# Optimization experiments

Measured on AMD Instinct MI355X. Metric: run time of the kernel, lower is better.

The kernel has to match this reference:

```python
import jax, jax.numpy as jnp
import numpy as np

N_NODES = 50000


def sage_conv(x, edge_index, W_l, b_l, W_r):
    # PyG SAGEConv (mean aggr): out_i = lin_l(mean_{j->i} x_j) + lin_r(x_i)
    src, dst = edge_index[0], edge_index[1]
    msgs = x[src]                                        # [E, C] gather
    summed = jax.ops.segment_sum(msgs, dst, num_segments=N_NODES)  # [N, C]
    deg = jax.ops.segment_sum(jnp.ones((edge_index.shape[1],), x.dtype), dst,
                              num_segments=N_NODES)
    mean = summed / jnp.maximum(deg, 1.0)[:, None]
    return mean @ W_l + b_l + x @ W_r


def setup_inputs() -> dict:
    key = jax.random.key(0)
    ks = jax.random.split(key, 12)
    E, EL, C, X = 800000, 1000000, 128, 384
    return {
        "x": jax.random.normal(ks[0], (N_NODES, X), jnp.float32),
        "edge_index": jax.random.randint(ks[1], (2, E), 0, N_NODES),
        "edge_label_index": jax.random.randint(ks[2], (2, EL), 0, N_NODES),
        "W_lin": jax.random.normal(ks[3], (X, C), jnp.float32) * 0.05,
        "b_lin": jax.random.normal(ks[4], (C,), jnp.float32) * 0.05,
        "W1_l": jax.random.normal(ks[5], (C, C), jnp.float32) * 0.08,
        "b1": jax.random.normal(ks[6], (C,), jnp.float32) * 0.05,
        "W1_r": jax.random.normal(ks[7], (C, C), jnp.float32) * 0.08,
        "W2_l": jax.random.normal(ks[8], (C, C), jnp.float32) * 0.08,
        "b2": jax.random.normal(ks[9], (C,), jnp.float32) * 0.05,
        "W2_r": jax.random.normal(ks[10], (C, C), jnp.float32) * 0.08,
    }


def reference(x, edge_index, edge_label_index, W_lin, b_lin,
              W1_l, b1, W1_r, W2_l, b2, W2_r):
    h = x @ W_lin + b_lin                                # label_lin
    h = jax.nn.relu(sage_conv(h, edge_index, W1_l, b1, W1_r))
    h = sage_conv(h, edge_index, W2_l, b2, W2_r)
    # Classifier: dot product of head/tail node features per label edge
    head = h[edge_label_index[0]]
    tail = h[edge_label_index[1]]
    return (head * tail).sum(axis=-1)                    # [EL]
```

## Files before the change

kernel.cpp:

```cpp
#include <hip/hip_runtime.h>

#define NODES 50000
#define CH 128
#define ELLW 64

using frag_ab = __attribute__((ext_vector_type(8))) short;
using frag_cd = __attribute__((ext_vector_type(4))) float;

__device__ __forceinline__ float bf2f(ushort u) {
    union { unsigned u; float f; } v; v.u = ((unsigned)u) << 16; return v.f;
}
__device__ __forceinline__ ushort f2bf(float f) {
    union { float f; unsigned u; } v; v.f = f;
    unsigned r = v.u + 0x7fff + ((v.u >> 16) & 1);
    return (ushort)(r >> 16);
}

__global__ void prep_weights(const float* __restrict__ Wlin,
                             const float* __restrict__ W1l, const float* __restrict__ W1r,
                             const float* __restrict__ W2l, const float* __restrict__ W2r,
                             ushort* __restrict__ o0, ushort* __restrict__ o1,
                             ushort* __restrict__ o2, ushort* __restrict__ o3,
                             ushort* __restrict__ o4, int* __restrict__ deg) {
    int b = blockIdx.x;
    if (b >= 448) {
        int i = (b - 448) * 256 + threadIdx.y * 128 + threadIdx.x;
        if (i < NODES) deg[i] = 0;
        return;
    }
    const float* W; ushort* O; int K; int kb;
    if (b < 192) { W = Wlin; O = o0; K = 384; kb = b; }
    else {
        int j = (b - 192) >> 6; kb = (b - 192) & 63; K = 128;
        W = (j == 0) ? W1l : (j == 1) ? W1r : (j == 2) ? W2l : W2r;
        O = (j == 0) ? o1  : (j == 1) ? o2  : (j == 2) ? o3  : o4;
    }
    int k = kb * 2 + threadIdx.y;
    int n = threadIdx.x;
    if (k < K) O[(size_t)n * K + k] = f2bf(W[(size_t)k * 128 + n]);
}

__global__ __launch_bounds__(256) void lin_and_ell(
    const float* __restrict__ A, const ushort* __restrict__ Wt,
    const float* __restrict__ bias, ushort* __restrict__ out, int N, int GB,
    const int* __restrict__ ei, int E, int* __restrict__ deg, ushort* __restrict__ ell)
{
    __shared__ ushort As[128 * 32];
    __shared__ ushort Bs[128 * 32];
    if (blockIdx.x >= GB) {
        int e0 = ((blockIdx.x - GB) * 256 + threadIdx.x) * 4;
        if (e0 >= E) return;
        int s[4], dd[4], cnt;
        if (((E & 3) == 0) && (e0 + 3 < E)) {
            int4 sv = *(const int4*)(ei + e0);
            int4 dv = *(const int4*)(ei + E + e0);
            s[0] = sv.x; s[1] = sv.y; s[2] = sv.z; s[3] = sv.w;
            dd[0] = dv.x; dd[1] = dv.y; dd[2] = dv.z; dd[3] = dv.w;
            cnt = 4;
        } else {
            cnt = E - e0; if (cnt > 4) cnt = 4;
#pragma unroll
            for (int j = 0; j < 4; ++j) {
                int e = (j < cnt) ? e0 + j : e0;
                s[j] = ei[e]; dd[j] = ei[E + e];
            }
        }
#pragma unroll
        for (int j = 0; j < 4; ++j) {
            if (j < cnt) {
                int pos = atomicAdd(&deg[dd[j]], 1);
                if (pos < ELLW) ell[(size_t)dd[j] * ELLW + pos] = (ushort)s[j];
            }
        }
        return;
    }
    const int tid = threadIdx.x;
    const int lane = tid & 63;
    const int wave = tid >> 6;
    const int wr = wave >> 1, wc = wave & 1;
    const int row0 = blockIdx.x * 128;
    const int l15 = lane & 15, quad = lane >> 4;

    frag_cd acc[4][4];
#pragma unroll
    for (int i = 0; i < 4; ++i)
#pragma unroll
        for (int j = 0; j < 4; ++j) acc[i][j] = (frag_cd){0.f, 0.f, 0.f, 0.f};

#pragma unroll 1
    for (int k0 = 0; k0 < 384; k0 += 32) {
        __syncthreads();
#pragma unroll
        for (int i = 0; i < 4; ++i) {
            int e = i * 256 + tid;
            int r = e >> 3, q = e & 7;
            int gr = row0 + r; if (gr > N - 1) gr = N - 1;
            float4 v = *(const float4*)(A + (size_t)gr * 384 + k0 + q * 4);
            ushort4 o; o.x = f2bf(v.x); o.y = f2bf(v.y); o.z = f2bf(v.z); o.w = f2bf(v.w);
            *(ushort4*)(As + r * 32 + q * 4) = o;
        }
#pragma unroll
        for (int i = 0; i < 2; ++i) {
            int e = i * 256 + tid;
            uint4 v = *(const uint4*)(Wt + (size_t)(e >> 2) * 384 + k0 + (e & 3) * 8);
            *(uint4*)(Bs + e * 8) = v;
        }
        __syncthreads();

        frag_ab a[4], b[4];
#pragma unroll
        for (int i = 0; i < 4; ++i)
            a[i] = *(const frag_ab*)(As + (wr * 64 + i * 16 + l15) * 32 + quad * 8);
#pragma unroll
        for (int j = 0; j < 4; ++j)
            b[j] = *(const frag_ab*)(Bs + (wc * 64 + j * 16 + l15) * 32 + quad * 8);
#pragma unroll
        for (int i = 0; i < 4; ++i)
#pragma unroll
            for (int j = 0; j < 4; ++j)
                acc[i][j] = __builtin_amdgcn_mfma_f32_16x16x32_bf16(a[i], b[j], acc[i][j], 0, 0, 0);
    }

#pragma unroll
    for (int i = 0; i < 4; ++i)
#pragma unroll
        for (int r = 0; r < 4; ++r) {
            int row = row0 + wr * 64 + i * 16 + quad * 4 + r;
            if (row < N)
#pragma unroll
                for (int j = 0; j < 4; ++j) {
                    int col = wc * 64 + j * 16 + l15;
                    out[(size_t)row * 128 + col] = f2bf(acc[i][j][r] + bias[col]);
                }
        }
}

__device__ __forceinline__ void acc8(float* acc, uint4 v) {
    acc[0] += bf2f((ushort)(v.x & 0xffff)); acc[1] += bf2f((ushort)(v.x >> 16));
    acc[2] += bf2f((ushort)(v.y & 0xffff)); acc[3] += bf2f((ushort)(v.y >> 16));
    acc[4] += bf2f((ushort)(v.z & 0xffff)); acc[5] += bf2f((ushort)(v.z >> 16));
    acc[6] += bf2f((ushort)(v.w & 0xffff)); acc[7] += bf2f((ushort)(v.w >> 16));
}

template <bool RELU>
__global__ __launch_bounds__(256) void agg_gemm(
    const ushort* __restrict__ h, const ushort* __restrict__ ell,
    const int* __restrict__ deg,
    const ushort* __restrict__ Wtl, const ushort* __restrict__ Wtr,
    const float* __restrict__ bias, ushort* __restrict__ out, int N)
{
    __shared__ ushort Ms[64 * 128];
    __shared__ ushort As[64 * 32];
    __shared__ ushort Bs[128 * 32];
    const int tid = threadIdx.x;
    const int lane = tid & 63;
    const int wave = tid >> 6;
    const int row0 = blockIdx.x * 64;
    const int g = lane >> 4;
    const int q = lane & 15;

#pragma unroll 1
    for (int it = 0; it < 4; ++it) {
        int r = (wave << 4) + (it << 2) + g;
        int node = row0 + r;
        int nd = node < N ? node : N - 1;
        const ushort* erow = ell + (size_t)nd * ELLW;
        int d = deg[nd];
        int dc = d < ELLW ? d : ELLW;
        float acc[8];
#pragma unroll
        for (int k = 0; k < 8; ++k) acc[k] = 0.f;
        int n = 0;
        for (; n + 4 <= dc; n += 4) {
            ushort4 iv = *(const ushort4*)(erow + n);
            uint4 v0 = *(const uint4*)(h + (size_t)iv.x * CH + q * 8);
            uint4 v1 = *(const uint4*)(h + (size_t)iv.y * CH + q * 8);
            uint4 v2 = *(const uint4*)(h + (size_t)iv.z * CH + q * 8);
            uint4 v3 = *(const uint4*)(h + (size_t)iv.w * CH + q * 8);
            acc8(acc, v0); acc8(acc, v1); acc8(acc, v2); acc8(acc, v3);
        }
        for (; n < dc; ++n) {
            uint4 v0 = *(const uint4*)(h + (size_t)erow[n] * CH + q * 8);
            acc8(acc, v0);
        }
        float inv = 1.f / fmaxf((float)d, 1.f);
        uint4 o;
        o.x = ((uint)f2bf(acc[1] * inv) << 16) | (uint)f2bf(acc[0] * inv);
        o.y = ((uint)f2bf(acc[3] * inv) << 16) | (uint)f2bf(acc[2] * inv);
        o.z = ((uint)f2bf(acc[5] * inv) << 16) | (uint)f2bf(acc[4] * inv);
        o.w = ((uint)f2bf(acc[7] * inv) << 16) | (uint)f2bf(acc[6] * inv);
        int chunk = q ^ (r & 7);
        *(uint4*)(Ms + r * 128 + chunk * 8) = o;
    }

    const int wr = wave >> 1, wc = wave & 1;
    const int l15 = q, quad = g;

    frag_cd acc2[2][4];
#pragma unroll
    for (int i = 0; i < 2; ++i)
#pragma unroll
        for (int j = 0; j < 4; ++j) acc2[i][j] = (frag_cd){0.f, 0.f, 0.f, 0.f};

#pragma unroll 1
    for (int part = 0; part < 2; ++part) {
        const ushort* Wt = part ? Wtr : Wtl;
#pragma unroll 1
        for (int k0 = 0; k0 < 128; k0 += 32) {
            __syncthreads();
            if (part) {
                int rr = tid >> 2, kq = tid & 3;
                int gr = row0 + rr; if (gr > N - 1) gr = N - 1;
                uint4 v = *(const uint4*)(h + (size_t)gr * CH + k0 + kq * 8);
                *(uint4*)(As + rr * 32 + ((kq ^ (rr & 3)) * 8)) = v;
            }
#pragma unroll
            for (int i2 = 0; i2 < 2; ++i2) {
                int e = i2 * 256 + tid;
                int br = e >> 2, bk = e & 3;
                uint4 v = *(const uint4*)(Wt + (size_t)br * 128 + k0 + bk * 8);
                *(uint4*)(Bs + br * 32 + ((bk ^ (br & 3)) * 8)) = v;
            }
            __syncthreads();

            frag_ab a[2], b[4];
#pragma unroll
            for (int i = 0; i < 2; ++i) {
                int ar = wr * 32 + i * 16 + l15;
                if (part) {
                    a[i] = *(const frag_ab*)(As + ar * 32 + ((quad ^ (ar & 3)) * 8));
                } else {
                    int ch = ((k0 >> 3) + quad) ^ (ar & 7);
                    a[i] = *(const frag_ab*)(Ms + ar * 128 + ch * 8);
                }
            }
#pragma unroll
            for (int j = 0; j < 4; ++j) {
                int br = wc * 64 + j * 16 + l15;
                b[j] = *(const frag_ab*)(Bs + br * 32 + ((quad ^ (br & 3)) * 8));
            }
#pragma unroll
            for (int i = 0; i < 2; ++i)
#pragma unroll
                for (int j = 0; j < 4; ++j)
                    acc2[i][j] = __builtin_amdgcn_mfma_f32_16x16x32_bf16(a[i], b[j], acc2[i][j], 0, 0, 0);
        }
    }

#pragma unroll
    for (int i = 0; i < 2; ++i)
#pragma unroll
        for (int rr = 0; rr < 4; ++rr) {
            int row = row0 + wr * 32 + i * 16 + quad * 4 + rr;
            if (row < N)
#pragma unroll
                for (int j = 0; j < 4; ++j) {
                    int col = wc * 64 + j * 16 + l15;
                    float v = acc2[i][j][rr] + bias[col];
                    if (RELU) v = fmaxf(v, 0.f);
                    out[(size_t)row * 128 + col] = f2bf(v);
                }
        }
}

__device__ __forceinline__ float dot8(uint4 va, uint4 vb) {
    float p = 0.f;
    p += bf2f((ushort)(va.x & 0xffff)) * bf2f((ushort)(vb.x & 0xffff));
    p += bf2f((ushort)(va.x >> 16))    * bf2f((ushort)(vb.x >> 16));
    p += bf2f((ushort)(va.y & 0xffff)) * bf2f((ushort)(vb.y & 0xffff));
    p += bf2f((ushort)(va.y >> 16))    * bf2f((ushort)(vb.y >> 16));
    p += bf2f((ushort)(va.z & 0xffff)) * bf2f((ushort)(vb.z & 0xffff));
    p += bf2f((ushort)(va.z >> 16))    * bf2f((ushort)(vb.z >> 16));
    p += bf2f((ushort)(va.w & 0xffff)) * bf2f((ushort)(vb.w & 0xffff));
    p += bf2f((ushort)(va.w >> 16))    * bf2f((ushort)(vb.w >> 16));
    return p;
}

__global__ __launch_bounds__(256) void classify_bf(
    const ushort* __restrict__ h2, const int* __restrict__ eli,
    int EL, float* __restrict__ out) {
    int gt = blockIdx.x * blockDim.x + threadIdx.x;
    int g0 = (gt >> 4) * 8;
    int lane = gt & 15;
    if (g0 >= EL) return;
    bool full = (g0 + 7 < EL);
    int ha[8], ta[8];
    if (full) {
        int4 h0 = *(const int4*)(eli + g0);
        int4 h1 = *(const int4*)(eli + g0 + 4);
        int4 t0 = *(const int4*)(eli + EL + g0);
        int4 t1 = *(const int4*)(eli + EL + g0 + 4);
        ha[0] = h0.x; ha[1] = h0.y; ha[2] = h0.z; ha[3] = h0.w;
        ha[4] = h1.x; ha[5] = h1.y; ha[6] = h1.z; ha[7] = h1.w;
        ta[0] = t0.x; ta[1] = t0.y; ta[2] = t0.z; ta[3] = t0.w;
        ta[4] = t1.x; ta[5] = t1.y; ta[6] = t1.z; ta[7] = t1.w;
    } else {
#pragma unroll
        for (int j = 0; j < 8; ++j) {
            int gj = (g0 + j < EL) ? g0 + j : EL - 1;
            ha[j] = eli[gj];
            ta[j] = eli[EL + gj];
        }
    }
    uint4 va[8], vb[8];
#pragma unroll
    for (int j = 0; j < 8; ++j) {
        va[j] = *((const uint4*)(h2 + (size_t)ha[j] * CH) + lane);
        vb[j] = *((const uint4*)(h2 + (size_t)ta[j] * CH) + lane);
    }
    float p[8];
#pragma unroll
    for (int j = 0; j < 8; ++j) p[j] = dot8(va[j], vb[j]);
#pragma unroll
    for (int s = 8; s >= 1; s >>= 1) {
#pragma unroll
        for (int j = 0; j < 8; ++j) p[j] += __shfl_down(p[j], s, 16);
    }
    if (lane == 0) {
        if (full) {
            *(float4*)(out + g0)     = make_float4(p[0], p[1], p[2], p[3]);
            *(float4*)(out + g0 + 4) = make_float4(p[4], p[5], p[6], p[7]);
        } else {
#pragma unroll
            for (int j = 0; j < 8; ++j)
                if (g0 + j < EL) out[g0 + j] = p[j];
        }
    }
}

extern "C" void kernel_launch(void* const* d_in, const int* in_sizes, int n_in,
                              void* d_out, int out_size, void* d_ws, size_t ws_size,
                              hipStream_t stream) {
    const float* x     = (const float*)d_in[0];
    const int*   ei    = (const int*)d_in[1];
    const int*   eli   = (const int*)d_in[2];
    const float* W_lin = (const float*)d_in[3];
    const float* b_lin = (const float*)d_in[4];
    const float* W1l   = (const float*)d_in[5];
    const float* b1    = (const float*)d_in[6];
    const float* W1r   = (const float*)d_in[7];
    const float* W2l   = (const float*)d_in[8];
    const float* b2    = (const float*)d_in[9];
    const float* W2r   = (const float*)d_in[10];
    float* out = (float*)d_out;

    const int E  = in_sizes[1] / 2;
    const int EL = in_sizes[2] / 2;
    const int N  = NODES;

    char* ws = (char*)d_ws;
    size_t off = 0;
    auto alloc = [&](size_t bytes) -> void* {
        void* p = ws + off;
        off += (bytes + 255) & ~(size_t)255;
        return p;
    };
    ushort* n0    = (ushort*)alloc((size_t)N * CH * sizeof(ushort));
    ushort* n1    = (ushort*)alloc((size_t)N * CH * sizeof(ushort));
    ushort* n2    = (ushort*)alloc((size_t)N * CH * sizeof(ushort));
    ushort* WtLin = (ushort*)alloc((size_t)CH * 384 * sizeof(ushort));
    ushort* Wt1l  = (ushort*)alloc((size_t)CH * CH * sizeof(ushort));
    ushort* Wt1r  = (ushort*)alloc((size_t)CH * CH * sizeof(ushort));
    ushort* Wt2l  = (ushort*)alloc((size_t)CH * CH * sizeof(ushort));
    ushort* Wt2r  = (ushort*)alloc((size_t)CH * CH * sizeof(ushort));
    int* deg = (int*)alloc((size_t)N * sizeof(int));
    ushort* ell = (ushort*)alloc((size_t)N * ELLW * sizeof(ushort));
    (void)ws_size; (void)n_in; (void)out_size;

    const int GB128 = (N + 127) / 128;
    const int GB64  = (N + 63) / 64;
    const int EB4   = (E + 1023) / 1024;

    prep_weights<<<dim3(644), dim3(128, 2), 0, stream>>>(
        W_lin, W1l, W1r, W2l, W2r, WtLin, Wt1l, Wt1r, Wt2l, Wt2r, deg);

    lin_and_ell<<<dim3(GB128 + EB4), dim3(256), 0, stream>>>(
        x, WtLin, b_lin, n0, N, GB128, ei, E, deg, ell);

    agg_gemm<true><<<dim3(GB64), dim3(256), 0, stream>>>(
        n0, ell, deg, Wt1l, Wt1r, b1, n2, N);

    agg_gemm<false><<<dim3(GB64), dim3(256), 0, stream>>>(
        n2, ell, deg, Wt2l, Wt2r, b2, n1, N);

    long long groups = ((long long)EL + 7) / 8;
    long long cls_threads = groups * 16;
    classify_bf<<<dim3((int)((cls_threads + 255) / 256)), dim3(256), 0, stream>>>(
        n1, eli, EL, out);
}
```

Before: 301.1 us.

## Pad degree counters to 64B stride and stage full weight matrices in LDS

The degree counters are now spaced 16 ints apart, so atomics on neighbouring destination nodes land on separate cache lines instead of contending on the same one. The aggregate+GEMM kernel now loads the whole 128x128 left weight into LDS once and runs the K loop with no barriers. It then reloads the right weight whole and streams only the self-feature tiles. In exchange LDS per block grows to roughly 52KB, which can reduce occupancy, and the degree array becomes 16x larger with strided reads in the gather phase.

```diff
diff --git a/kernel.cpp b/kernel.cpp
--- a/kernel.cpp
+++ b/kernel.cpp
@@ -21,11 +21,11 @@
                              const float* __restrict__ W2l, const float* __restrict__ W2r,
                              ushort* __restrict__ o0, ushort* __restrict__ o1,
                              ushort* __restrict__ o2, ushort* __restrict__ o3,
-                             ushort* __restrict__ o4, int* __restrict__ deg) {
+                             ushort* __restrict__ o4, int* __restrict__ degs) {
     int b = blockIdx.x;
     if (b >= 448) {
         int i = (b - 448) * 256 + threadIdx.y * 128 + threadIdx.x;
-        if (i < NODES) deg[i] = 0;
+        if (i < NODES) degs[i << 4] = 0;
         return;
     }
     const float* W; ushort* O; int K; int kb;
@@ -43,7 +43,7 @@
 __global__ __launch_bounds__(256) void lin_and_ell(
     const float* __restrict__ A, const ushort* __restrict__ Wt,
     const float* __restrict__ bias, ushort* __restrict__ out, int N, int GB,
-    const int* __restrict__ ei, int E, int* __restrict__ deg, ushort* __restrict__ ell)
+    const int* __restrict__ ei, int E, int* __restrict__ degs, ushort* __restrict__ ell)
 {
     __shared__ ushort As[128 * 32];
     __shared__ ushort Bs[128 * 32];
@@ -68,7 +68,7 @@
 #pragma unroll
         for (int j = 0; j < 4; ++j) {
             if (j < cnt) {
-                int pos = atomicAdd(&deg[dd[j]], 1);
+                int pos = atomicAdd(&degs[dd[j] << 4], 1);
                 if (pos < ELLW) ell[(size_t)dd[j] * ELLW + pos] = (ushort)s[j];
             }
         }
@@ -143,15 +143,15 @@
 }
 
 template <bool RELU>
-__global__ __launch_bounds__(256) void agg_gemm(
+__global__ __launch_bounds__(256) void agg_gemm2(
     const ushort* __restrict__ h, const ushort* __restrict__ ell,
-    const int* __restrict__ deg,
+    const int* __restrict__ degs,
     const ushort* __restrict__ Wtl, const ushort* __restrict__ Wtr,
     const float* __restrict__ bias, ushort* __restrict__ out, int N)
 {
     __shared__ ushort Ms[64 * 128];
     __shared__ ushort As[64 * 32];
-    __shared__ ushort Bs[128 * 32];
+    __shared__ ushort Bs[128 * 128];
     const int tid = threadIdx.x;
     const int lane = tid & 63;
     const int wave = tid >> 6;
@@ -159,13 +159,21 @@
     const int g = lane >> 4;
     const int q = lane & 15;
 
+#pragma unroll
+    for (int i = 0; i < 8; ++i) {
+        int e = i * 256 + tid;
+        int br = e >> 4, c = e & 15;
+        uint4 v = *(const uint4*)(Wtl + (size_t)br * 128 + c * 8);
+        *(uint4*)(Bs + br * 128 + ((c ^ (br & 7)) * 8)) = v;
+    }
+
 #pragma unroll 1
     for (int it = 0; it < 4; ++it) {
         int r = (wave << 4) + (it << 2) + g;
         int node = row0 + r;
         int nd = node < N ? node : N - 1;
         const ushort* erow = ell + (size_t)nd * ELLW;
-        int d = deg[nd];
+        int d = degs[nd << 4];
         int dc = d < ELLW ? d : ELLW;
         float acc[8];
 #pragma unroll
@@ -192,6 +200,7 @@
         int chunk = q ^ (r & 7);
         *(uint4*)(Ms + r * 128 + chunk * 8) = o;
     }
+    __syncthreads();
 
     const int wr = wave >> 1, wc = wave & 1;
     const int l15 = q, quad = g;
@@ -203,48 +212,62 @@
         for (int j = 0; j < 4; ++j) acc2[i][j] = (frag_cd){0.f, 0.f, 0.f, 0.f};
 
 #pragma unroll 1
-    for (int part = 0; part < 2; ++part) {
-        const ushort* Wt = part ? Wtr : Wtl;
+    for (int k0 = 0; k0 < 128; k0 += 32) {
+        frag_ab a[2], b[4];
+#pragma unroll
+        for (int i = 0; i < 2; ++i) {
+            int ar = wr * 32 + i * 16 + l15;
+            int c = ((k0 >> 3) + quad) ^ (ar & 7);
+            a[i] = *(const frag_ab*)(Ms + ar * 128 + c * 8);
+        }
+#pragma unroll
+        for (int j = 0; j < 4; ++j) {
+            int br = wc * 64 + j * 16 + l15;
+            int c = ((k0 >> 3) + quad) ^ (br & 7);
+            b[j] = *(const frag_ab*)(Bs + br * 128 + c * 8);
+        }
+#pragma unroll
+        for (int i = 0; i < 2; ++i)
+#pragma unroll
+            for (int j = 0; j < 4; ++j)
+                acc2[i][j] = __builtin_amdgcn_mfma_f32_16x16x32_bf16(a[i], b[j], acc2[i][j], 0, 0, 0);
+    }
+    __syncthreads();
+
+#pragma unroll
+    for (int i = 0; i < 8; ++i) {
+        int e = i * 256 + tid;
+        int br = e >> 4, c = e & 15;
+        uint4 v = *(const uint4*)(Wtr + (size_t)br * 128 + c * 8);
+        *(uint4*)(Bs + br * 128 + ((c ^ (br & 7)) * 8)) = v;
+    }
+
 #pragma unroll 1
-        for (int k0 = 0; k0 < 128; k0 += 32) {
-            __syncthreads();
-            if (part) {
-                int rr = tid >> 2, kq = tid & 3;
-                int gr = row0 + rr; if (gr > N - 1) gr = N - 1;
-                uint4 v = *(const uint4*)(h + (size_t)gr * CH + k0 + kq * 8);
-                *(uint4*)(As + rr * 32 + ((kq ^ (rr & 3)) * 8)) = v;
-            }
-#pragma unroll
-            for (int i2 = 0; i2 < 2; ++i2) {
-                int e = i2 * 256 + tid;
-                int br = e >> 2, bk = e & 3;
-                uint4 v = *(const uint4*)(Wt + (size_t)br * 128 + k0 + bk * 8);
-                *(uint4*)(Bs + br * 32 + ((bk ^ (br & 3)) * 8)) = v;
-            }
-            __syncthreads();
-
-            frag_ab a[2], b[4];
-#pragma unroll
-            for (int i = 0; i < 2; ++i) {
-                int ar = wr * 32 + i * 16 + l15;
-                if (part) {
-                    a[i] = *(const frag_ab*)(As + ar * 32 + ((quad ^ (ar & 3)) * 8));
-                } else {
-                    int ch = ((k0 >> 3) + quad) ^ (ar & 7);
-                    a[i] = *(const frag_ab*)(Ms + ar * 128 + ch * 8);
-                }
-            }
-#pragma unroll
-            for (int j = 0; j < 4; ++j) {
-                int br = wc * 64 + j * 16 + l15;
-                b[j] = *(const frag_ab*)(Bs + br * 32 + ((quad ^ (br & 3)) * 8));
-            }
-#pragma unroll
-            for (int i = 0; i < 2; ++i)
-#pragma unroll
-                for (int j = 0; j < 4; ++j)
-                    acc2[i][j] = __builtin_amdgcn_mfma_f32_16x16x32_bf16(a[i], b[j], acc2[i][j], 0, 0, 0);
-        }
+    for (int k0 = 0; k0 < 128; k0 += 32) {
+        int r = tid >> 2, kq = tid & 3;
+        int gr = row0 + r; if (gr > N - 1) gr = N - 1;
+        uint4 v = *(const uint4*)(h + (size_t)gr * CH + k0 + kq * 8);
+        __syncthreads();
+        *(uint4*)(As + r * 32 + ((kq ^ (r & 3)) * 8)) = v;
+        __syncthreads();
+
+        frag_ab a[2], b[4];
+#pragma unroll
+        for (int i = 0; i < 2; ++i) {
+            int ar = wr * 32 + i * 16 + l15;
+            a[i] = *(const frag_ab*)(As + ar * 32 + ((quad ^ (ar & 3)) * 8));
+        }
+#pragma unroll
+        for (int j = 0; j < 4; ++j) {
+            int br = wc * 64 + j * 16 + l15;
+            int c = ((k0 >> 3) + quad) ^ (br & 7);
+            b[j] = *(const frag_ab*)(Bs + br * 128 + c * 8);
+        }
+#pragma unroll
+        for (int i = 0; i < 2; ++i)
+#pragma unroll
+            for (int j = 0; j < 4; ++j)
+                acc2[i][j] = __builtin_amdgcn_mfma_f32_16x16x32_bf16(a[i], b[j], acc2[i][j], 0, 0, 0);
     }
 
 #pragma unroll
@@ -363,25 +386,25 @@
     ushort* Wt1r  = (ushort*)alloc((size_t)CH * CH * sizeof(ushort));
     ushort* Wt2l  = (ushort*)alloc((size_t)CH * CH * sizeof(ushort));
     ushort* Wt2r  = (ushort*)alloc((size_t)CH * CH * sizeof(ushort));
-    int* deg = (int*)alloc((size_t)N * sizeof(int));
+    int* degs = (int*)alloc((size_t)N * 16 * sizeof(int));
     ushort* ell = (ushort*)alloc((size_t)N * ELLW * sizeof(ushort));
     (void)ws_size; (void)n_in; (void)out_size;
 
     const int GB128 = (N + 127) / 128;
-    const int GB64  = (N + 63) / 64;
     const int EB4   = (E + 1023) / 1024;
+    const int AB64  = (N + 63) / 64;
 
     prep_weights<<<dim3(644), dim3(128, 2), 0, stream>>>(
-        W_lin, W1l, W1r, W2l, W2r, WtLin, Wt1l, Wt1r, Wt2l, Wt2r, deg);
+        W_lin, W1l, W1r, W2l, W2r, WtLin, Wt1l, Wt1r, Wt2l, Wt2r, degs);
 
     lin_and_ell<<<dim3(GB128 + EB4), dim3(256), 0, stream>>>(
-        x, WtLin, b_lin, n0, N, GB128, ei, E, deg, ell);
-
-    agg_gemm<true><<<dim3(GB64), dim3(256), 0, stream>>>(
-        n0, ell, deg, Wt1l, Wt1r, b1, n2, N);
-
-    agg_gemm<false><<<dim3(GB64), dim3(256), 0, stream>>>(
-        n2, ell, deg, Wt2l, Wt2r, b2, n1, N);
+        x, WtLin, b_lin, n0, N, GB128, ei, E, degs, ell);
+
+    agg_gemm2<true><<<dim3(AB64), dim3(256), 0, stream>>>(
+        n0, ell, degs, Wt1l, Wt1r, b1, n2, N);
+
+    agg_gemm2<false><<<dim3(AB64), dim3(256), 0, stream>>>(
+        n2, ell, degs, Wt2l, Wt2r, b2, n1, N);
 
     long long groups = ((long long)EL + 7) / 8;
     long long cls_threads = groups * 16;
```

After: 340.4 us. 13.1% more time.
